# Optimization experiments

Hardware: AMD Instinct MI355X
Metric: run time of the kernel (lower is better)

Reference implementation:

```python
import jax, jax.numpy as jnp
import numpy as np

NUM_NODES_FEAT = 400   # per-graph node count == input feature dim (fMRI ROIs)
F1 = 256
F2 = 256
NUM_GRAPHS = 256
N_TOTAL = NUM_GRAPHS * NUM_NODES_FEAT  # 102400 nodes
E_TOTAL = 4096000                      # ~40 avg degree


def setup_inputs() -> dict:
    key = jax.random.key(0)
    ks = jax.random.split(key, 8)
    x = jax.random.normal(ks[0], (N_TOTAL, NUM_NODES_FEAT), dtype=jnp.float32)
    edge_index = jax.random.randint(ks[1], (2, E_TOTAL), 0, N_TOTAL, dtype=jnp.int64)
    # PyG-style block-diagonal batch vector: 400 nodes per graph
    batch = jnp.repeat(jnp.arange(NUM_GRAPHS, dtype=jnp.int64), NUM_NODES_FEAT)
    # learned params (xavier-ish scale)
    def xavier(k, shape):
        fan_in, fan_out = shape[0], shape[1]
        s = jnp.sqrt(6.0 / (fan_in + fan_out))
        return jax.random.uniform(k, shape, jnp.float32, -s, s)
    W1 = xavier(ks[2], (NUM_NODES_FEAT, F1))
    b1 = jax.random.uniform(ks[3], (F1,), jnp.float32)
    W2 = xavier(ks[4], (F1, F2))
    b2 = jax.random.uniform(ks[5], (F2,), jnp.float32)
    Wm = xavier(ks[6], (2 * F2, 2))   # meanmax readout -> 2*f2 input
    bm = jax.random.uniform(ks[7], (2,), jnp.float32)
    return {"x": x, "edge_index": edge_index, "batch": batch,
            "num_graphs": NUM_GRAPHS,
            "W1": W1, "b1": b1, "W2": W2, "b2": b2, "Wm": Wm, "bm": bm}


def _gcn_conv(x, W, b, src, dst, deg_inv_sqrt, n):
    # PyG GCNConv: linear transform, then deg^{-1/2}-normalized scatter-add
    h = x @ W                                   # [N, f_out]
    norm = deg_inv_sqrt[src] * deg_inv_sqrt[dst]  # [E+N]
    msgs = h[src] * norm[:, None]               # gather + scale
    out = jax.ops.segment_sum(msgs, dst, num_segments=n)
    return out + b


def reference(x, edge_index, batch, num_graphs, W1, b1, W2, b2, Wm, bm):
    n = x.shape[0]
    loops = jnp.arange(n, dtype=edge_index.dtype)
    src = jnp.concatenate([edge_index[0], loops])  # add self-loops (PyG default)
    dst = jnp.concatenate([edge_index[1], loops])
    deg = jax.ops.segment_sum(jnp.ones_like(dst, dtype=x.dtype), dst, num_segments=n)
    deg_inv_sqrt = jnp.where(deg > 0, jax.lax.rsqrt(deg), 0.0)

    h = _gcn_conv(x, W1, b1, src, dst, deg_inv_sqrt, n)
    h = jax.nn.relu(h)
    # F.dropout(training=False) -> identity in eval mode
    h = _gcn_conv(h, W2, b2, src, dst, deg_inv_sqrt, n)

    # meanmax graph readout over batch segments
    g_sum = jax.ops.segment_sum(h, batch, num_segments=num_graphs)
    cnt = jax.ops.segment_sum(jnp.ones((n,), h.dtype), batch, num_segments=num_graphs)
    g_mean = g_sum / jnp.maximum(cnt, 1.0)[:, None]
    g_max = jax.ops.segment_max(h, batch, num_segments=num_graphs)
    g = jnp.concatenate([g_mean, g_max], axis=-1)  # [G, 2*f2]
    return g @ Wm + bm                             # [G, 2]
```

## Files before the change

kernel.cpp:

```cpp
#include <hip/hip_runtime.h>
#include <hip/hip_bf16.h>

#define N_NODES 102400
#define FEAT    400
#define F1      256
#define E_EDGES 4096000
#define NUM_G   256
#define NPG     400
#define NSLICE  8
#define NODES_PER_SLICE (NPG / NSLICE)

#define NBIN    400
#define BINCAP  12288
#define EPB     4096
#define BIN_BLOCKS (E_EDGES / EPB)

typedef __attribute__((ext_vector_type(8))) short bfrag;
typedef __attribute__((ext_vector_type(4))) float ffrag;
typedef __attribute__((ext_vector_type(4))) short s4;

__device__ inline short f2b(float f) {
    __hip_bfloat16 h = __float2bfloat16(f);
    return *reinterpret_cast<short*>(&h);
}

#define ACC(uu) { auto vl = __builtin_amdgcn_cvt_pk_f32_fp8(uu, false); \
                  auto vh = __builtin_amdgcn_cvt_pk_f32_fp8(uu, true);  \
                  a0 += vl[0]; a1 += vl[1]; a2 += vh[0]; a3 += vh[1]; }

__global__ __launch_bounds__(256) void k_bin(const int* __restrict__ ei,
                                             int* __restrict__ binfill,
                                             int2* __restrict__ binbuf) {
    __shared__ int h[NBIN], base[NBIN], cur[NBIN];
    const int t  = threadIdx.x;
    const int e0 = blockIdx.x * EPB;
    for (int b = t; b < NBIN; b += 256) h[b] = 0;
    __syncthreads();
#pragma unroll 4
    for (int k = 0; k < 16; ++k) {
        int d = ei[E_EDGES + e0 + k * 256 + t];
        atomicAdd(&h[d >> 8], 1);
    }
    __syncthreads();
    for (int b = t; b < NBIN; b += 256) {
        base[b] = atomicAdd(&binfill[b], h[b]);
        cur[b]  = 0;
    }
    __syncthreads();
#pragma unroll 4
    for (int k = 0; k < 16; ++k) {
        int e = e0 + k * 256 + t;
        int s = ei[e];
        int d = ei[E_EDGES + e];
        int bin = d >> 8;
        int idx = base[bin] + atomicAdd(&cur[bin], 1);
        if (idx < BINCAP) binbuf[(size_t)bin * BINCAP + idx] = make_int2(s, d);
    }
}

__global__ __launch_bounds__(256) void k_bcnt(const int* __restrict__ binfill,
                                              const int2* __restrict__ binbuf,
                                              int* __restrict__ cnt,
                                              float* __restrict__ dis) {
    __shared__ int h[256];
    const int b = blockIdx.x, t = threadIdx.x;
    h[t] = 0;
    __syncthreads();
    int n = binfill[b]; if (n > BINCAP) n = BINCAP;
    const int2* p = binbuf + (size_t)b * BINCAP;
    for (int i = t; i < n; i += 256) atomicAdd(&h[p[i].y & 255], 1);
    __syncthreads();
    int node = b * 256 + t;
    cnt[node] = h[t];
    dis[node] = rsqrtf((float)(h[t] + 1));
}

__global__ __launch_bounds__(1024) void k_scan1(const int* __restrict__ cnt,
                                                int* __restrict__ part,
                                                int* __restrict__ bsum) {
    __shared__ int s[1024];
    int t = threadIdx.x, b = blockIdx.x;
    int gid = b * 1024 + t;
    s[t] = cnt[gid];
    __syncthreads();
    for (int off = 1; off < 1024; off <<= 1) {
        int v = (t >= off) ? s[t - off] : 0;
        __syncthreads();
        s[t] += v;
        __syncthreads();
    }
    part[gid] = s[t];
    if (t == 1023) bsum[b] = s[t];
}

__global__ void k_scan2(int* __restrict__ bsum) {
    if (threadIdx.x == 0) {
        int run = 0;
        for (int i = 0; i < N_NODES / 1024; ++i) {
            int v = bsum[i]; bsum[i] = run; run += v;
        }
    }
}

__global__ __launch_bounds__(1024) void k_scan3(const int* __restrict__ cnt,
                                                const int* __restrict__ part,
                                                const int* __restrict__ bsum,
                                                int* __restrict__ row_start) {
    int t = threadIdx.x, b = blockIdx.x;
    int gid = b * 1024 + t;
    int inc = part[gid];
    row_start[gid] = inc - cnt[gid] + bsum[b];
    if (gid == N_NODES - 1) row_start[N_NODES] = inc + bsum[b];
}

__global__ __launch_bounds__(256) void k_bfill(const int* __restrict__ binfill,
                                               const int2* __restrict__ binbuf,
                                               const int* __restrict__ row_start,
                                               int* __restrict__ csr) {
    __shared__ int rs[256], cur[256];
    const int b = blockIdx.x, t = threadIdx.x;
    rs[t]  = row_start[b * 256 + t];
    cur[t] = 0;
    __syncthreads();
    int n = binfill[b]; if (n > BINCAP) n = BINCAP;
    const int2* p = binbuf + (size_t)b * BINCAP;
    for (int i = t; i < n; i += 256) {
        int2 e = p[i];
        int dl = e.y & 255;
        int pos = atomicAdd(&cur[dl], 1);
        csr[rs[dl] + pos] = e.x;
    }
}

__global__ __launch_bounds__(256) void k_cvt_w(const float* __restrict__ W,
                                               short* __restrict__ Wt,
                                               int Kreal, int Kpad) {
    int idx = blockIdx.x * 256 + threadIdx.x;
    if (idx >= 256 * Kpad) return;
    int n = idx / Kpad, k = idx - n * Kpad;
    float v = (k < Kreal) ? W[(size_t)k * 256 + n] : 0.f;
    Wt[idx] = f2b(v);
}

template<bool AF32>
__global__ __launch_bounds__(256) void k_mm(const void* __restrict__ Ap,
                                            const short* __restrict__ Wt,
                                            const float* __restrict__ dis,
                                            int Kreal, int Kpad,
                                            unsigned char* __restrict__ Cp) {
    __shared__ short As[128][40];
    __shared__ short Bs[128][40];
    const int t    = threadIdx.x;
    const int lane = t & 63;
    const int w    = t >> 6;
    const int wm   = w >> 1, wn = w & 1;
    const int m0   = blockIdx.x * 128;
    const int n0   = blockIdx.y * 128;

    const int sr = t >> 1;
    const int sh = (t & 1) * 16;

    ffrag acc[4][4];
#pragma unroll
    for (int i = 0; i < 4; ++i)
#pragma unroll
        for (int j = 0; j < 4; ++j) {
            ffrag z = {0.f, 0.f, 0.f, 0.f};
            acc[i][j] = z;
        }

    const int rl = lane & 15;
    const int kc = (lane >> 4) * 8;

    for (int k0 = 0; k0 < Kpad; k0 += 32) {
        short av[16], bv[16];
        if constexpr (AF32) {
            const float* A = (const float*)Ap;
            const float* arow = A + (size_t)(m0 + sr) * Kreal + k0 + sh;
#pragma unroll
            for (int c = 0; c < 4; ++c) {
                float4 v;
                if (k0 + sh + c * 4 < Kreal) v = *(const float4*)(arow + c * 4);
                else                         v = make_float4(0.f, 0.f, 0.f, 0.f);
                av[c * 4 + 0] = f2b(v.x);
                av[c * 4 + 1] = f2b(v.y);
                av[c * 4 + 2] = f2b(v.z);
                av[c * 4 + 3] = f2b(v.w);
            }
        } else {
            const short* A = (const short*)Ap;
            const short* arow = A + (size_t)(m0 + sr) * Kpad + k0 + sh;
            *(bfrag*)&av[0] = *(const bfrag*)arow;
            *(bfrag*)&av[8] = *(const bfrag*)(arow + 8);
        }
        const short* brow = Wt + (size_t)(n0 + sr) * Kpad + k0 + sh;
        *(bfrag*)&bv[0] = *(const bfrag*)brow;
        *(bfrag*)&bv[8] = *(const bfrag*)(brow + 8);

        __syncthreads();
        *(bfrag*)&As[sr][sh]     = *(bfrag*)&av[0];
        *(bfrag*)&As[sr][sh + 8] = *(bfrag*)&av[8];
        *(bfrag*)&Bs[sr][sh]     = *(bfrag*)&bv[0];
        *(bfrag*)&Bs[sr][sh + 8] = *(bfrag*)&bv[8];
        __syncthreads();

        bfrag a[4], b[4];
#pragma unroll
        for (int i = 0; i < 4; ++i) a[i] = *(const bfrag*)&As[wm * 64 + i * 16 + rl][kc];
#pragma unroll
        for (int j = 0; j < 4; ++j) b[j] = *(const bfrag*)&Bs[wn * 64 + j * 16 + rl][kc];
#pragma unroll
        for (int i = 0; i < 4; ++i)
#pragma unroll
            for (int j = 0; j < 4; ++j)
                acc[i][j] = __builtin_amdgcn_mfma_f32_16x16x32_bf16(a[i], b[j], acc[i][j], 0, 0, 0);
    }

    const int rh = lane >> 4;
    float scale[4][4];
#pragma unroll
    for (int i = 0; i < 4; ++i)
#pragma unroll
        for (int q = 0; q < 4; ++q)
            scale[i][q] = dis[m0 + wm * 64 + i * 16 + rh * 4 + q];

#pragma unroll
    for (int i = 0; i < 4; ++i)
#pragma unroll
        for (int j = 0; j < 4; ++j) {
            int col  = n0 + wn * 64 + j * 16 + rl;
            int rowb = m0 + wm * 64 + i * 16 + rh * 4;
#pragma unroll
            for (int q = 0; q < 4; ++q) {
                float v = acc[i][j][q] * scale[i][q];
                int p = __builtin_amdgcn_cvt_pk_fp8_f32(v, 0.f, 0, false);
                Cp[(size_t)(rowb + q) * 256 + col] = (unsigned char)(p & 0xff);
            }
        }
}

__global__ __launch_bounds__(256) void k_agg8(const unsigned int* __restrict__ h8,
                                              const float* __restrict__ dis,
                                              const int* __restrict__ row_start,
                                              const int* __restrict__ csr,
                                              const float* __restrict__ bias,
                                              short* __restrict__ out) {
    const int w = threadIdx.x >> 6;
    const int t = threadIdx.x & 63;
    const int i = blockIdx.x * 4 + w;
    float di = dis[i];
    unsigned int u = h8[(size_t)i * 64 + t];
    auto lo = __builtin_amdgcn_cvt_pk_f32_fp8(u, false);
    auto hi = __builtin_amdgcn_cvt_pk_f32_fp8(u, true);
    float a0 = lo[0], a1 = lo[1], a2 = hi[0], a3 = hi[1];

    const int beg = row_start[i], end = row_start[i + 1];
    const int* row = csr + beg;
    const int n = end - beg;
    int j = 0;
    for (; j + 4 <= n; j += 4) {
        int s0 = row[j], s1 = row[j + 1], s2 = row[j + 2], s3 = row[j + 3];
        unsigned int u0 = h8[(size_t)s0 * 64 + t];
        unsigned int u1 = h8[(size_t)s1 * 64 + t];
        unsigned int u2 = h8[(size_t)s2 * 64 + t];
        unsigned int u3 = h8[(size_t)s3 * 64 + t];
        ACC(u0) ACC(u1) ACC(u2) ACC(u3)
    }
    for (; j < n; ++j) {
        unsigned int uv = h8[(size_t)row[j] * 64 + t];
        ACC(uv)
    }
    float4 bb = *(const float4*)(bias + t * 4);
    s4 o;
    o[0] = f2b(fmaxf(fmaf(di, a0, bb.x), 0.f));
    o[1] = f2b(fmaxf(fmaf(di, a1, bb.y), 0.f));
    o[2] = f2b(fmaxf(fmaf(di, a2, bb.z), 0.f));
    o[3] = f2b(fmaxf(fmaf(di, a3, bb.w), 0.f));
    *(s4*)(out + (size_t)i * 256 + t * 4) = o;
}

__global__ __launch_bounds__(256) void k_agg2f(const unsigned int* __restrict__ h8,
                                               const float* __restrict__ dis,
                                               const int* __restrict__ row_start,
                                               const int* __restrict__ csr,
                                               const float* __restrict__ bias,
                                               float* __restrict__ partial) {
    const int g     = blockIdx.x;
    const int slice = blockIdx.y;
    const int t     = threadIdx.x;
    const int w     = t >> 6;
    const int lane  = t & 63;

    float4 bb = *(const float4*)(bias + lane * 4);
    float sm[4] = {0.f, 0.f, 0.f, 0.f};
    float mx[4] = {-3.402823466e38f, -3.402823466e38f, -3.402823466e38f, -3.402823466e38f};

    const int r0 = slice * NODES_PER_SLICE;
    for (int r = r0 + w; r < r0 + NODES_PER_SLICE; r += 4) {
        int i = g * NPG + r;
        float di = dis[i];
        unsigned int u = h8[(size_t)i * 64 + lane];
        auto lo = __builtin_amdgcn_cvt_pk_f32_fp8(u, false);
        auto hi = __builtin_amdgcn_cvt_pk_f32_fp8(u, true);
        float a0 = lo[0], a1 = lo[1], a2 = hi[0], a3 = hi[1];

        const int beg = row_start[i], end = row_start[i + 1];
        const int* row = csr + beg;
        const int n = end - beg;
        int j = 0;
        for (; j + 4 <= n; j += 4) {
            int s0 = row[j], s1 = row[j + 1], s2 = row[j + 2], s3 = row[j + 3];
            unsigned int u0 = h8[(size_t)s0 * 64 + lane];
            unsigned int u1 = h8[(size_t)s1 * 64 + lane];
            unsigned int u2 = h8[(size_t)s2 * 64 + lane];
            unsigned int u3 = h8[(size_t)s3 * 64 + lane];
            ACC(u0) ACC(u1) ACC(u2) ACC(u3)
        }
        for (; j < n; ++j) {
            unsigned int uv = h8[(size_t)row[j] * 64 + lane];
            ACC(uv)
        }
        float h0 = fmaf(di, a0, bb.x);
        float h1 = fmaf(di, a1, bb.y);
        float h2 = fmaf(di, a2, bb.z);
        float h3 = fmaf(di, a3, bb.w);
        sm[0] += h0; sm[1] += h1; sm[2] += h2; sm[3] += h3;
        mx[0] = fmaxf(mx[0], h0); mx[1] = fmaxf(mx[1], h1);
        mx[2] = fmaxf(mx[2], h2); mx[3] = fmaxf(mx[3], h3);
    }

    __shared__ float ls[4][256];
    __shared__ float lm[4][256];
#pragma unroll
    for (int k = 0; k < 4; ++k) {
        ls[w][lane * 4 + k] = sm[k];
        lm[w][lane * 4 + k] = mx[k];
    }
    __syncthreads();
    if (w == 0) {
        float* base = partial + ((size_t)g * NSLICE + slice) * 512;
#pragma unroll
        for (int k = 0; k < 4; ++k) {
            int f = lane * 4 + k;
            base[f]       = ls[0][f] + ls[1][f] + ls[2][f] + ls[3][f];
            base[256 + f] = fmaxf(fmaxf(lm[0][f], lm[1][f]), fmaxf(lm[2][f], lm[3][f]));
        }
    }
}

__global__ __launch_bounds__(256) void k_final(const float* __restrict__ partial,
                                               const float* __restrict__ Wm,
                                               const float* __restrict__ bm,
                                               float* __restrict__ out) {
    int g = blockIdx.x, t = threadIdx.x;
    const float* pg = partial + (size_t)g * NSLICE * 512;
    float sum = 0.f, mxv = -3.402823466e38f;
#pragma unroll
    for (int s = 0; s < NSLICE; ++s) {
        sum += pg[s * 512 + t];
        mxv = fmaxf(mxv, pg[s * 512 + 256 + t]);
    }
    float mean = sum * (1.0f / NPG);
    float p0 = mean * Wm[t * 2 + 0] + mxv * Wm[(256 + t) * 2 + 0];
    float p1 = mean * Wm[t * 2 + 1] + mxv * Wm[(256 + t) * 2 + 1];
    __shared__ float2 red[256];
    red[t] = make_float2(p0, p1);
    __syncthreads();
    for (int s2 = 128; s2 > 0; s2 >>= 1) {
        if (t < s2) {
            red[t].x += red[t + s2].x;
            red[t].y += red[t + s2].y;
        }
        __syncthreads();
    }
    if (t == 0) {
        out[g * 2 + 0] = red[0].x + bm[0];
        out[g * 2 + 1] = red[0].y + bm[1];
    }
}

extern "C" void kernel_launch(void* const* d_in, const int* in_sizes, int n_in,
                              void* d_out, int out_size, void* d_ws, size_t ws_size,
                              hipStream_t stream) {
    const float* x  = (const float*)d_in[0];
    const int*   ei = (const int*)d_in[1];
    const float* W1 = (const float*)d_in[4];
    const float* b1 = (const float*)d_in[5];
    const float* W2 = (const float*)d_in[6];
    const float* b2 = (const float*)d_in[7];
    const float* Wm = (const float*)d_in[8];
    const float* bm = (const float*)d_in[9];
    float* out = (float*)d_out;

    char* ws = (char*)d_ws;
    size_t off = 0;
    auto alloc = [&](size_t bytes) {
        void* p = ws + off;
        off = (off + bytes + 255) & ~(size_t)255;
        return p;
    };
    int*   binfill   = (int*)alloc((size_t)NBIN * 4);
    int2*  binbuf    = (int2*)alloc((size_t)NBIN * BINCAP * 8);
    int*   cnt       = (int*)alloc((size_t)N_NODES * 4);
    int*   part      = (int*)alloc((size_t)N_NODES * 4);
    int*   bsum      = (int*)alloc(512);
    int*   row_start = (int*)alloc((size_t)(N_NODES + 1) * 4);
    float* dis       = (float*)alloc((size_t)N_NODES * 4);
    int*   csr       = (int*)alloc((size_t)E_EDGES * 4);
    short* Wt1       = (short*)alloc((size_t)256 * 416 * 2);
    short* Wt2       = (short*)alloc((size_t)256 * 256 * 2);
    unsigned char* P8 = (unsigned char*)alloc((size_t)N_NODES * F1);
    short* Pb        = (short*)alloc((size_t)N_NODES * F1 * 2);
    float* partialb  = (float*)alloc((size_t)NUM_G * NSLICE * 512 * 4);

    hipMemsetAsync(binfill, 0, (size_t)NBIN * 4, stream);
    k_bin<<<BIN_BLOCKS, 256, 0, stream>>>(ei, binfill, binbuf);
    k_bcnt<<<NBIN, 256, 0, stream>>>(binfill, binbuf, cnt, dis);
    k_scan1<<<N_NODES / 1024, 1024, 0, stream>>>(cnt, part, bsum);
    k_scan2<<<1, 64, 0, stream>>>(bsum);
    k_scan3<<<N_NODES / 1024, 1024, 0, stream>>>(cnt, part, bsum, row_start);
    k_bfill<<<NBIN, 256, 0, stream>>>(binfill, binbuf, row_start, csr);

    k_cvt_w<<<(256 * 416 + 255) / 256, 256, 0, stream>>>(W1, Wt1, 400, 416);
    k_cvt_w<<<(256 * 256 + 255) / 256, 256, 0, stream>>>(W2, Wt2, 256, 256);

    dim3 gg(N_NODES / 128, 2);
    k_mm<true><<<gg, 256, 0, stream>>>((const void*)x, Wt1, dis, 400, 416, P8);
    k_agg8<<<N_NODES / 4, 256, 0, stream>>>((const unsigned int*)P8, dis, row_start,
                                            csr, b1, Pb);
    k_mm<false><<<gg, 256, 0, stream>>>((const void*)Pb, Wt2, dis, 256, 256, P8);
    k_agg2f<<<dim3(NUM_G, NSLICE), 256, 0, stream>>>((const unsigned int*)P8, dis,
                                                     row_start, csr, b2, partialb);
    k_final<<<NUM_G, 256, 0, stream>>>(partialb, Wm, bm, out);
}
```

Baseline: 605.1 us.

## Fuse preprocessing kernels, merge CSR fill with first GEMM, deepen gather unroll

The weight conversions are folded into the binning launch. The three-kernel global scan is replaced by a small per-bin prefix scan followed by an in-block scan inside the degree-count kernel. The CSR fill and the first GEMM now run as one heterogeneous launch, which is valid because the GEMM needs only dis and not the CSR. The aggregation loops gather 8 neighbours per iteration to keep more loads in flight. The aim is to cut launch count and serial gaps between small kernels. The cost is more register pressure in the aggregation kernels and mixed block shapes within one grid.

```diff
diff --git a/kernel.cpp b/kernel.cpp
--- a/kernel.cpp
+++ b/kernel.cpp
@@ -14,6 +14,9 @@
 #define BINCAP  12288
 #define EPB     4096
 #define BIN_BLOCKS (E_EDGES / EPB)
+#define CVT1_BLOCKS 416
+#define CVT2_BLOCKS 256
+#define CVT_BLOCKS  (CVT1_BLOCKS + CVT2_BLOCKS)
 
 typedef __attribute__((ext_vector_type(8))) short bfrag;
 typedef __attribute__((ext_vector_type(4))) float ffrag;
@@ -28,41 +31,76 @@
                   auto vh = __builtin_amdgcn_cvt_pk_f32_fp8(uu, true);  \
                   a0 += vl[0]; a1 += vl[1]; a2 += vh[0]; a3 += vh[1]; }
 
-__global__ __launch_bounds__(256) void k_bin(const int* __restrict__ ei,
-                                             int* __restrict__ binfill,
-                                             int2* __restrict__ binbuf) {
-    __shared__ int h[NBIN], base[NBIN], cur[NBIN];
-    const int t  = threadIdx.x;
-    const int e0 = blockIdx.x * EPB;
-    for (int b = t; b < NBIN; b += 256) h[b] = 0;
-    __syncthreads();
+__global__ __launch_bounds__(256) void k_binA(const int* __restrict__ ei,
+                                              int* __restrict__ binfill,
+                                              int2* __restrict__ binbuf,
+                                              const float* __restrict__ W1,
+                                              const float* __restrict__ W2,
+                                              short* __restrict__ Wt1,
+                                              short* __restrict__ Wt2) {
+    const int t = threadIdx.x;
+    if (blockIdx.x < BIN_BLOCKS) {
+        __shared__ int h[NBIN], base[NBIN], cur[NBIN];
+        const int e0 = blockIdx.x * EPB;
+        for (int b = t; b < NBIN; b += 256) h[b] = 0;
+        __syncthreads();
 #pragma unroll 4
-    for (int k = 0; k < 16; ++k) {
-        int d = ei[E_EDGES + e0 + k * 256 + t];
-        atomicAdd(&h[d >> 8], 1);
-    }
-    __syncthreads();
-    for (int b = t; b < NBIN; b += 256) {
-        base[b] = atomicAdd(&binfill[b], h[b]);
-        cur[b]  = 0;
-    }
-    __syncthreads();
+        for (int k = 0; k < 16; ++k) {
+            int d = ei[E_EDGES + e0 + k * 256 + t];
+            atomicAdd(&h[d >> 8], 1);
+        }
+        __syncthreads();
+        for (int b = t; b < NBIN; b += 256) {
+            base[b] = atomicAdd(&binfill[b], h[b]);
+            cur[b]  = 0;
+        }
+        __syncthreads();
 #pragma unroll 4
-    for (int k = 0; k < 16; ++k) {
-        int e = e0 + k * 256 + t;
-        int s = ei[e];
-        int d = ei[E_EDGES + e];
-        int bin = d >> 8;
-        int idx = base[bin] + atomicAdd(&cur[bin], 1);
-        if (idx < BINCAP) binbuf[(size_t)bin * BINCAP + idx] = make_int2(s, d);
-    }
+        for (int k = 0; k < 16; ++k) {
+            int e = e0 + k * 256 + t;
+            int s = ei[e];
+            int d = ei[E_EDGES + e];
+            int bin = d >> 8;
+            int idx = base[bin] + atomicAdd(&cur[bin], 1);
+            if (idx < BINCAP) binbuf[(size_t)bin * BINCAP + idx] = make_int2(s, d);
+        }
+    } else {
+        int cb = blockIdx.x - BIN_BLOCKS;
+        if (cb < CVT1_BLOCKS) {
+            int idx = cb * 256 + t;
+            int n = idx / 416, k = idx - n * 416;
+            float v = (k < 400) ? W1[(size_t)k * 256 + n] : 0.f;
+            Wt1[idx] = f2b(v);
+        } else {
+            int idx = (cb - CVT1_BLOCKS) * 256 + t;
+            int n = idx >> 8, k = idx & 255;
+            Wt2[idx] = f2b(W2[(size_t)k * 256 + n]);
+        }
+    }
+}
+
+__global__ __launch_bounds__(512) void k_binscan(const int* __restrict__ binfill,
+                                                 int* __restrict__ binbase) {
+    __shared__ int s[512];
+    int t = threadIdx.x;
+    int v = (t < NBIN) ? binfill[t] : 0;
+    s[t] = v;
+    __syncthreads();
+    for (int off = 1; off < 512; off <<= 1) {
+        int u = (t >= off) ? s[t - off] : 0;
+        __syncthreads();
+        s[t] += u;
+        __syncthreads();
+    }
+    if (t < NBIN) binbase[t] = s[t] - v;
 }
 
 __global__ __launch_bounds__(256) void k_bcnt(const int* __restrict__ binfill,
+                                              const int* __restrict__ binbase,
                                               const int2* __restrict__ binbuf,
-                                              int* __restrict__ cnt,
+                                              int* __restrict__ row_start,
                                               float* __restrict__ dis) {
-    __shared__ int h[256];
+    __shared__ int h[256], sc[256];
     const int b = blockIdx.x, t = threadIdx.x;
     h[t] = 0;
     __syncthreads();
@@ -70,95 +108,38 @@
     const int2* p = binbuf + (size_t)b * BINCAP;
     for (int i = t; i < n; i += 256) atomicAdd(&h[p[i].y & 255], 1);
     __syncthreads();
+    int deg = h[t];
+    sc[t] = deg;
+    __syncthreads();
+    for (int off = 1; off < 256; off <<= 1) {
+        int u = (t >= off) ? sc[t - off] : 0;
+        __syncthreads();
+        sc[t] += u;
+        __syncthreads();
+    }
     int node = b * 256 + t;
-    cnt[node] = h[t];
-    dis[node] = rsqrtf((float)(h[t] + 1));
-}
-
-__global__ __launch_bounds__(1024) void k_scan1(const int* __restrict__ cnt,
-                                                int* __restrict__ part,
-                                                int* __restrict__ bsum) {
-    __shared__ int s[1024];
-    int t = threadIdx.x, b = blockIdx.x;
-    int gid = b * 1024 + t;
-    s[t] = cnt[gid];
-    __syncthreads();
-    for (int off = 1; off < 1024; off <<= 1) {
-        int v = (t >= off) ? s[t - off] : 0;
-        __syncthreads();
-        s[t] += v;
-        __syncthreads();
-    }
-    part[gid] = s[t];
-    if (t == 1023) bsum[b] = s[t];
-}
-
-__global__ void k_scan2(int* __restrict__ bsum) {
-    if (threadIdx.x == 0) {
-        int run = 0;
-        for (int i = 0; i < N_NODES / 1024; ++i) {
-            int v = bsum[i]; bsum[i] = run; run += v;
-        }
-    }
-}
-
-__global__ __launch_bounds__(1024) void k_scan3(const int* __restrict__ cnt,
-                                                const int* __restrict__ part,
-                                                const int* __restrict__ bsum,
-                                                int* __restrict__ row_start) {
-    int t = threadIdx.x, b = blockIdx.x;
-    int gid = b * 1024 + t;
-    int inc = part[gid];
-    row_start[gid] = inc - cnt[gid] + bsum[b];
-    if (gid == N_NODES - 1) row_start[N_NODES] = inc + bsum[b];
-}
-
-__global__ __launch_bounds__(256) void k_bfill(const int* __restrict__ binfill,
-                                               const int2* __restrict__ binbuf,
-                                               const int* __restrict__ row_start,
-                                               int* __restrict__ csr) {
-    __shared__ int rs[256], cur[256];
-    const int b = blockIdx.x, t = threadIdx.x;
-    rs[t]  = row_start[b * 256 + t];
-    cur[t] = 0;
-    __syncthreads();
-    int n = binfill[b]; if (n > BINCAP) n = BINCAP;
-    const int2* p = binbuf + (size_t)b * BINCAP;
-    for (int i = t; i < n; i += 256) {
-        int2 e = p[i];
-        int dl = e.y & 255;
-        int pos = atomicAdd(&cur[dl], 1);
-        csr[rs[dl] + pos] = e.x;
-    }
-}
-
-__global__ __launch_bounds__(256) void k_cvt_w(const float* __restrict__ W,
-                                               short* __restrict__ Wt,
-                                               int Kreal, int Kpad) {
-    int idx = blockIdx.x * 256 + threadIdx.x;
-    if (idx >= 256 * Kpad) return;
-    int n = idx / Kpad, k = idx - n * Kpad;
-    float v = (k < Kreal) ? W[(size_t)k * 256 + n] : 0.f;
-    Wt[idx] = f2b(v);
+    row_start[node] = binbase[b] + sc[t] - deg;
+    dis[node] = rsqrtf((float)(deg + 1));
+    if (b == NBIN - 1 && t == 255) row_start[N_NODES] = binbase[b] + sc[t];
 }
 
 template<bool AF32>
-__global__ __launch_bounds__(256) void k_mm(const void* __restrict__ Ap,
-                                            const short* __restrict__ Wt,
-                                            const float* __restrict__ dis,
-                                            int Kreal, int Kpad,
-                                            unsigned char* __restrict__ Cp) {
+__device__ void mm_body(int bm, int bn,
+                        const void* __restrict__ Ap,
+                        const short* __restrict__ Wt,
+                        const float* __restrict__ dis,
+                        int Kreal, int Kpad,
+                        unsigned char* __restrict__ Cp) {
     __shared__ short As[128][40];
     __shared__ short Bs[128][40];
     const int t    = threadIdx.x;
     const int lane = t & 63;
     const int w    = t >> 6;
     const int wm   = w >> 1, wn = w & 1;
-    const int m0   = blockIdx.x * 128;
-    const int n0   = blockIdx.y * 128;
-
-    const int sr = t >> 1;
-    const int sh = (t & 1) * 16;
+    const int m0   = bm * 128;
+    const int n0   = bn * 128;
+    const int sr   = t >> 1;
+    const int sh   = (t & 1) * 16;
 
     ffrag acc[4][4];
 #pragma unroll
@@ -239,6 +220,41 @@
         }
 }
 
+__global__ __launch_bounds__(256) void k_fillmm(const int* __restrict__ binfill,
+                                                const int2* __restrict__ binbuf,
+                                                const int* __restrict__ row_start,
+                                                int* __restrict__ csr,
+                                                const float* __restrict__ x,
+                                                const short* __restrict__ Wt1,
+                                                const float* __restrict__ dis,
+                                                unsigned char* __restrict__ P8) {
+    if (blockIdx.x < NBIN) {
+        __shared__ int rs[256], cur[256];
+        const int b = blockIdx.x, t = threadIdx.x;
+        rs[t]  = row_start[b * 256 + t];
+        cur[t] = 0;
+        __syncthreads();
+        int n = binfill[b]; if (n > BINCAP) n = BINCAP;
+        const int2* p = binbuf + (size_t)b * BINCAP;
+        for (int i = t; i < n; i += 256) {
+            int2 e = p[i];
+            int dl = e.y & 255;
+            int pos = atomicAdd(&cur[dl], 1);
+            csr[rs[dl] + pos] = e.x;
+        }
+    } else {
+        int bx = blockIdx.x - NBIN;
+        mm_body<true>(bx >> 1, bx & 1, (const void*)x, Wt1, dis, 400, 416, P8);
+    }
+}
+
+__global__ __launch_bounds__(256) void k_mm2(const short* __restrict__ Pb,
+                                             const short* __restrict__ Wt2,
+                                             const float* __restrict__ dis,
+                                             unsigned char* __restrict__ P8) {
+    mm_body<false>(blockIdx.x, blockIdx.y, (const void*)Pb, Wt2, dis, 256, 256, P8);
+}
+
 __global__ __launch_bounds__(256) void k_agg8(const unsigned int* __restrict__ h8,
                                               const float* __restrict__ dis,
                                               const int* __restrict__ row_start,
@@ -258,13 +274,19 @@
     const int* row = csr + beg;
     const int n = end - beg;
     int j = 0;
+    for (; j + 8 <= n; j += 8) {
+        unsigned int uu[8];
+#pragma unroll
+        for (int k = 0; k < 8; ++k) uu[k] = h8[(size_t)row[j + k] * 64 + t];
+#pragma unroll
+        for (int k = 0; k < 8; ++k) ACC(uu[k])
+    }
     for (; j + 4 <= n; j += 4) {
-        int s0 = row[j], s1 = row[j + 1], s2 = row[j + 2], s3 = row[j + 3];
-        unsigned int u0 = h8[(size_t)s0 * 64 + t];
-        unsigned int u1 = h8[(size_t)s1 * 64 + t];
-        unsigned int u2 = h8[(size_t)s2 * 64 + t];
-        unsigned int u3 = h8[(size_t)s3 * 64 + t];
-        ACC(u0) ACC(u1) ACC(u2) ACC(u3)
+        unsigned int uu[4];
+#pragma unroll
+        for (int k = 0; k < 4; ++k) uu[k] = h8[(size_t)row[j + k] * 64 + t];
+#pragma unroll
+        for (int k = 0; k < 4; ++k) ACC(uu[k])
     }
     for (; j < n; ++j) {
         unsigned int uv = h8[(size_t)row[j] * 64 + t];
@@ -308,13 +330,19 @@
         const int* row = csr + beg;
         const int n = end - beg;
         int j = 0;
+        for (; j + 8 <= n; j += 8) {
+            unsigned int uu[8];
+#pragma unroll
+            for (int k = 0; k < 8; ++k) uu[k] = h8[(size_t)row[j + k] * 64 + lane];
+#pragma unroll
+            for (int k = 0; k < 8; ++k) ACC(uu[k])
+        }
         for (; j + 4 <= n; j += 4) {
-            int s0 = row[j], s1 = row[j + 1], s2 = row[j + 2], s3 = row[j + 3];
-            unsigned int u0 = h8[(size_t)s0 * 64 + lane];
-            unsigned int u1 = h8[(size_t)s1 * 64 + lane];
-            unsigned int u2 = h8[(size_t)s2 * 64 + lane];
-            unsigned int u3 = h8[(size_t)s3 * 64 + lane];
-            ACC(u0) ACC(u1) ACC(u2) ACC(u3)
+            unsigned int uu[4];
+#pragma unroll
+            for (int k = 0; k < 4; ++k) uu[k] = h8[(size_t)row[j + k] * 64 + lane];
+#pragma unroll
+            for (int k = 0; k < 4; ++k) ACC(uu[k])
         }
         for (; j < n; ++j) {
             unsigned int uv = h8[(size_t)row[j] * 64 + lane];
@@ -400,10 +428,8 @@
         return p;
     };
     int*   binfill   = (int*)alloc((size_t)NBIN * 4);
+    int*   binbase   = (int*)alloc((size_t)NBIN * 4);
     int2*  binbuf    = (int2*)alloc((size_t)NBIN * BINCAP * 8);
-    int*   cnt       = (int*)alloc((size_t)N_NODES * 4);
-    int*   part      = (int*)alloc((size_t)N_NODES * 4);
-    int*   bsum      = (int*)alloc(512);
     int*   row_start = (int*)alloc((size_t)(N_NODES + 1) * 4);
     float* dis       = (float*)alloc((size_t)N_NODES * 4);
     int*   csr       = (int*)alloc((size_t)E_EDGES * 4);
@@ -414,21 +440,15 @@
     float* partialb  = (float*)alloc((size_t)NUM_G * NSLICE * 512 * 4);
 
     hipMemsetAsync(binfill, 0, (size_t)NBIN * 4, stream);
-    k_bin<<<BIN_BLOCKS, 256, 0, stream>>>(ei, binfill, binbuf);
-    k_bcnt<<<NBIN, 256, 0, stream>>>(binfill, binbuf, cnt, dis);
-    k_scan1<<<N_NODES / 1024, 1024, 0, stream>>>(cnt, part, bsum);
-    k_scan2<<<1, 64, 0, stream>>>(bsum);
-    k_scan3<<<N_NODES / 1024, 1024, 0, stream>>>(cnt, part, bsum, row_start);
-    k_bfill<<<NBIN, 256, 0, stream>>>(binfill, binbuf, row_start, csr);
-
-    k_cvt_w<<<(256 * 416 + 255) / 256, 256, 0, stream>>>(W1, Wt1, 400, 416);
-    k_cvt_w<<<(256 * 256 + 255) / 256, 256, 0, stream>>>(W2, Wt2, 256, 256);
-
-    dim3 gg(N_NODES / 128, 2);
-    k_mm<true><<<gg, 256, 0, stream>>>((const void*)x, Wt1, dis, 400, 416, P8);
+    k_binA<<<BIN_BLOCKS + CVT_BLOCKS, 256, 0, stream>>>(ei, binfill, binbuf,
+                                                        W1, W2, Wt1, Wt2);
+    k_binscan<<<1, 512, 0, stream>>>(binfill, binbase);
+    k_bcnt<<<NBIN, 256, 0, stream>>>(binfill, binbase, binbuf, row_start, dis);
+    k_fillmm<<<NBIN + 1600, 256, 0, stream>>>(binfill, binbuf, row_start, csr,
+                                              x, Wt1, dis, P8);
     k_agg8<<<N_NODES / 4, 256, 0, stream>>>((const unsigned int*)P8, dis, row_start,
                                             csr, b1, Pb);
-    k_mm<false><<<gg, 256, 0, stream>>>((const void*)Pb, Wt2, dis, 256, 256, P8);
+    k_mm2<<<dim3(800, 2), 256, 0, stream>>>(Pb, Wt2, dis, P8);
     k_agg2f<<<dim3(NUM_G, NSLICE), 256, 0, stream>>>((const unsigned int*)P8, dis,
                                                      row_start, csr, b2, partialb);
     k_final<<<NUM_G, 256, 0, stream>>>(partialb, Wm, bm, out);
```

Measured after the change: 548.6 us. 1.1x faster.
